# Kernel tuning notes

Measured on AMD Instinct MI355X. Metric: run time of the kernel, lower is better.

The kernel has to match this reference:

```python
import jax, jax.numpy as jnp
import numpy as np
import math

B, N, IN_DIM, EMBED, HEADS = 1, 96, 128, 128, 4
HD = EMBED // HEADS  # head_dim = 32


def _layernorm(x, g, b, eps=1e-5):
    mu = jnp.mean(x, axis=-1, keepdims=True)
    var = jnp.var(x, axis=-1, keepdims=True)
    return (x - mu) * jax.lax.rsqrt(var + eps) * g + b


def setup_inputs() -> dict:
    key = jax.random.key(0)
    ks = jax.random.split(key, 3)
    x = jax.random.normal(ks[0], (B, N, N, IN_DIM), dtype=jnp.float32)
    W = jax.random.normal(ks[1], (IN_DIM, EMBED), dtype=jnp.float32) / math.sqrt(IN_DIM)
    b = jnp.zeros((EMBED,), jnp.float32)
    ln_g = jnp.ones((HD,), jnp.float32)
    ln_b = jnp.zeros((HD,), jnp.float32)
    Wf = jax.random.normal(ks[2], (IN_DIM + EMBED, EMBED), dtype=jnp.float32) / math.sqrt(IN_DIM + EMBED)
    bf = jnp.zeros((EMBED,), jnp.float32)
    ln2_g = jnp.ones((EMBED,), jnp.float32)
    ln2_b = jnp.zeros((EMBED,), jnp.float32)
    return {"x": x, "W": W, "b": b, "ln_g": ln_g, "ln_b": ln_b,
            "Wf": Wf, "bf": bf, "ln2_g": ln2_g, "ln2_b": ln2_b}


def reference(x, W, b, ln_g, ln_b, Wf, bf, ln2_g, ln2_b):
    # NOTE: original torch module shares ONE Linear across q/k/v1/v2 and ONE
    # LayerNorm across norms[0..2] (ModuleList([m]*k) aliases the module).
    Bq, Nq = x.shape[0], x.shape[1]
    p = (jnp.einsum('bxyi,ie->bxye', x, W) + b).reshape(Bq, Nq, Nq, HEADS, HD)
    pn = _layernorm(p, ln_g, ln_b)                         # q == k (shared params)
    scores = jnp.einsum('bxahd,bayhd->bxayh', pn, pn) / math.sqrt(HD)
    att = jax.nn.softmax(scores, axis=2)                   # softmax over a
    x_upd = jnp.einsum('bxahd,bayhd->bxayhd', p, p)        # v1 == v2 == p
    x_upd = _layernorm(x_upd, ln_g, ln_b)                  # shared norm params
    agg = jnp.einsum('bxayh,bxayhd->bxyhd', att, x_upd).reshape(Bq, Nq, Nq, EMBED)
    cat = jnp.concatenate([x, agg], axis=-1)
    out = jnp.einsum('bxyc,ce->bxye', cat, Wf) + bf
    return _layernorm(out, ln2_g, ln2_b)
```

## Files before the change

kernel.cpp:

```cpp
#include <hip/hip_runtime.h>
#include <math.h>

#define NTOK 96
#define EMBED 128
#define HEADS 4
#define HD 32
#define NROW (NTOK*NTOK)
#define YT 8
#define NYT (NTOK/YT)

__global__ __launch_bounds__(128) void k_proj(
    const float* __restrict__ x, const float* __restrict__ W,
    const float* __restrict__ b,
    float* __restrict__ pT, float* __restrict__ murT) {
  const int r0 = blockIdx.x * 4;
  const int X  = r0 / NTOK;
  const int y0 = r0 % NTOK;
  const int e  = threadIdx.x;
  __shared__ float xt[EMBED][4];
  #pragma unroll
  for (int k = 0; k < 4; ++k)
    xt[e][k] = x[(size_t)(r0 + k) * EMBED + e];
  __syncthreads();

  const float bias = b[e];
  float a0 = bias, a1 = bias, a2 = bias, a3 = bias;
  #pragma unroll 8
  for (int i = 0; i < EMBED; ++i) {
    const float wv = W[(size_t)i * EMBED + e];
    const float4 c = *(const float4*)&xt[i][0];
    a0 = fmaf(wv, c.x, a0); a1 = fmaf(wv, c.y, a1);
    a2 = fmaf(wv, c.z, a2); a3 = fmaf(wv, c.w, a3);
  }

  const int h = e >> 5;
  float accs[4] = {a0, a1, a2, a3};
  #pragma unroll
  for (int k = 0; k < 4; ++k) {
    pT[((size_t)(y0 + k) * NTOK + X) * EMBED + e] = accs[k];
    float s1 = accs[k], s2 = accs[k] * accs[k];
    #pragma unroll
    for (int m_ = 1; m_ < 32; m_ <<= 1) {
      s1 += __shfl_xor(s1, m_, 64);
      s2 += __shfl_xor(s2, m_, 64);
    }
    if ((e & 31) == 0) {
      const float mu = s1 * (1.f / HD);
      const float var = fmaxf(s2 * (1.f / HD) - mu * mu, 0.f);
      float2 v; v.x = mu; v.y = rsqrtf(var + 1e-5f);
      *(float2*)&murT[(((size_t)(y0 + k) * NTOK + X) * HEADS + h) * 2] = v;
    }
  }
}

__device__ __forceinline__ void sc_elem(float e, float f, float g, float b,
    float rE, float pE, float rF, float pF,
    float& s, float& m, float& q, float& t) {
  const float uE = fmaf(e, rE, -pE);
  const float en = fmaf(uE, g, b);
  const float uF = fmaf(f, rF, -pF);
  const float fn = fmaf(uF, g, b);
  s = fmaf(en, fn, s);
  t = e * f;
  m += t;
  q = fmaf(t, t, q);
}

#define SC_QUAD(E4, F4, G4, B4, T4) \
  sc_elem(E4.x, F4.x, G4.x, B4.x, rE, pE, rF, pF, s, m, q, T4.x); \
  sc_elem(E4.y, F4.y, G4.y, B4.y, rE, pE, rF, pF, s, m, q, T4.y); \
  sc_elem(E4.z, F4.z, G4.z, B4.z, rE, pE, rF, pF, s, m, q, T4.z); \
  sc_elem(E4.w, F4.w, G4.w, B4.w, rE, pE, rF, pF, s, m, q, T4.w);

#define AGG_QUAD(A4, T4) \
  A4.x = fmaf(w, T4.x, A4.x); A4.y = fmaf(w, T4.y, A4.y); \
  A4.z = fmaf(w, T4.z, A4.z); A4.w = fmaf(w, T4.w, A4.w);

#define SCALE_QUAD(A4) \
  A4.x *= scale; A4.y *= scale; A4.z *= scale; A4.w *= scale;

#define RED_QUAD(A4, MASK) \
  A4.x += __shfl_xor(A4.x, MASK, 64); A4.y += __shfl_xor(A4.y, MASK, 64); \
  A4.z += __shfl_xor(A4.z, MASK, 64); A4.w += __shfl_xor(A4.w, MASK, 64);

__global__ __launch_bounds__(256) void k_fused(
    const float* __restrict__ pT, const float* __restrict__ murT,
    const float* __restrict__ ln_g, const float* __restrict__ ln_b,
    const float* __restrict__ x, const float* __restrict__ Wf,
    const float* __restrict__ bf, const float* __restrict__ g2,
    const float* __restrict__ b2, float* __restrict__ out) {
  const int bid = blockIdx.x;
  const int X   = bid % NTOK;
  const int y0  = (bid / NTOK) * YT;

  const int tid = threadIdx.x;
  const int y   = tid >> 5;
  const int ds  = (tid >> 4) & 1;
  const int da  = tid & 15;
  const int yy  = y0 + y;
  const int eoff = ds * 16;

  __shared__ float e_sm[NTOK][36];
  __shared__ float mur_sm[NTOK][2];
  __shared__ float xt_sm[EMBED][12];
  __shared__ float agg_t[EMBED][12];
  __shared__ float g_sm[HD], b_sm[HD];
  __shared__ float red_sm[4][4][2];

  #pragma unroll
  for (int i = 0; i < 4; ++i) {
    const int g = tid + i * 256;
    const int yl = g >> 7, col = g & 127;
    xt_sm[col][yl] = x[((size_t)(X * NTOK + y0 + yl)) * EMBED + col];
  }
  if (tid < HD) { g_sm[tid] = ln_g[tid]; b_sm[tid] = ln_b[tid]; }

  for (int H = 0; H < HEADS; ++H) {
    __syncthreads();
    #pragma unroll
    for (int i = 0; i < 3; ++i) {
      const int g = tid + i * 256;
      const int a = g >> 3, qq = g & 7;
      *(float4*)&e_sm[a][qq * 4] =
          *(const float4*)&pT[((size_t)a * NTOK + X) * EMBED + H * HD + qq * 4];
    }
    if (tid < NTOK) {
      const float2 v = *(const float2*)&murT[(((size_t)tid * NTOK + X) * HEADS + H) * 2];
      mur_sm[tid][0] = v.x; mur_sm[tid][1] = v.y;
    }
    __syncthreads();

    const float4 g0 = *(const float4*)&g_sm[eoff];
    const float4 g1 = *(const float4*)&g_sm[eoff + 4];
    const float4 g2v = *(const float4*)&g_sm[eoff + 8];
    const float4 g3 = *(const float4*)&g_sm[eoff + 12];
    const float4 b0 = *(const float4*)&b_sm[eoff];
    const float4 b1 = *(const float4*)&b_sm[eoff + 4];
    const float4 b2v = *(const float4*)&b_sm[eoff + 8];
    const float4 b3 = *(const float4*)&b_sm[eoff + 12];

    const float* fbase = pT + (size_t)yy * NTOK * EMBED + H * HD + eoff;
    const float* mbase = murT + ((size_t)yy * NTOK * HEADS + H) * 2;

    float4 acc0 = {0,0,0,0}, acc1 = {0,0,0,0}, acc2 = {0,0,0,0}, acc3 = {0,0,0,0};
    float den = 0.f, cc = 0.f, mx = -1e30f;

    #pragma unroll 2
    for (int ia = 0; ia < 6; ++ia) {
      const int a = ia * 16 + da;
      const float4* fp = (const float4*)(fbase + (size_t)a * EMBED);
      const float4 f0 = fp[0], f1 = fp[1], f2 = fp[2], f3 = fp[3];
      const float2 mrF = *(const float2*)(mbase + (size_t)a * (HEADS * 2));
      const float muE = mur_sm[a][0], rE = mur_sm[a][1];
      const float rF = mrF.y;
      const float pE = muE * rE;
      const float pF = mrF.x * rF;
      const float4 e0 = *(const float4*)&e_sm[a][eoff];
      const float4 e1 = *(const float4*)&e_sm[a][eoff + 4];
      const float4 e2 = *(const float4*)&e_sm[a][eoff + 8];
      const float4 e3 = *(const float4*)&e_sm[a][eoff + 12];

      float s = 0.f, m = 0.f, q = 0.f;
      float4 t0, t1, t2, t3;
      SC_QUAD(e0, f0, g0, b0, t0);
      SC_QUAD(e1, f1, g1, b1, t1);
      SC_QUAD(e2, f2, g2v, b2v, t2);
      SC_QUAD(e3, f3, g3, b3, t3);

      s += __shfl_xor(s, 16, 64);
      m += __shfl_xor(m, 16, 64);
      q += __shfl_xor(q, 16, 64);

      const float mu = m * (1.f / HD);
      const float var = fmaxf(fmaf(-mu, mu, q * (1.f / HD)), 0.f);
      const float r = rsqrtf(var + 1e-5f);
      const float sc = s * 0.17677669529663687f;

      float mc = sc;
      mc = fmaxf(mc, __shfl_xor(mc, 1, 64));
      mc = fmaxf(mc, __shfl_xor(mc, 2, 64));
      mc = fmaxf(mc, __shfl_xor(mc, 4, 64));
      mc = fmaxf(mc, __shfl_xor(mc, 8, 64));
      const float nmx = fmaxf(mx, mc);
      const float scale = __expf(mx - nmx);
      mx = nmx;
      const float ex = __expf(sc - mx);
      const float w = ex * r;
      den = fmaf(den, scale, ex);
      cc  = fmaf(cc,  scale, w * mu);
      SCALE_QUAD(acc0); SCALE_QUAD(acc1); SCALE_QUAD(acc2); SCALE_QUAD(acc3);
      AGG_QUAD(acc0, t0);
      AGG_QUAD(acc1, t1);
      AGG_QUAD(acc2, t2);
      AGG_QUAD(acc3, t3);
    }

    #pragma unroll
    for (int mask = 1; mask <= 8; mask <<= 1) {
      den += __shfl_xor(den, mask, 64);
      cc  += __shfl_xor(cc,  mask, 64);
      RED_QUAD(acc0, mask);
      RED_QUAD(acc1, mask);
      RED_QUAD(acc2, mask);
      RED_QUAD(acc3, mask);
    }

    if (da == 0) {
      const float inv = 1.f / den;
      float ov[16];
      ov[0]  = fmaf(g0.x, (acc0.x - cc) * inv, b0.x);
      ov[1]  = fmaf(g0.y, (acc0.y - cc) * inv, b0.y);
      ov[2]  = fmaf(g0.z, (acc0.z - cc) * inv, b0.z);
      ov[3]  = fmaf(g0.w, (acc0.w - cc) * inv, b0.w);
      ov[4]  = fmaf(g1.x, (acc1.x - cc) * inv, b1.x);
      ov[5]  = fmaf(g1.y, (acc1.y - cc) * inv, b1.y);
      ov[6]  = fmaf(g1.z, (acc1.z - cc) * inv, b1.z);
      ov[7]  = fmaf(g1.w, (acc1.w - cc) * inv, b1.w);
      ov[8]  = fmaf(g2v.x, (acc2.x - cc) * inv, b2v.x);
      ov[9]  = fmaf(g2v.y, (acc2.y - cc) * inv, b2v.y);
      ov[10] = fmaf(g2v.z, (acc2.z - cc) * inv, b2v.z);
      ov[11] = fmaf(g2v.w, (acc2.w - cc) * inv, b2v.w);
      ov[12] = fmaf(g3.x, (acc3.x - cc) * inv, b3.x);
      ov[13] = fmaf(g3.y, (acc3.y - cc) * inv, b3.y);
      ov[14] = fmaf(g3.z, (acc3.z - cc) * inv, b3.z);
      ov[15] = fmaf(g3.w, (acc3.w - cc) * inv, b3.w);
      #pragma unroll
      for (int j = 0; j < 16; ++j)
        agg_t[H * HD + eoff + j][y] = ov[j];
    }
  }
  __syncthreads();

  const int e  = tid & 127;
  const int rh = tid >> 7;
  const float bias = bf[e];
  float acc4[4] = {bias, bias, bias, bias};

  #pragma unroll 8
  for (int i = 0; i < EMBED; ++i) {
    const float wv = Wf[(size_t)i * EMBED + e];
    const float4 c0 = *(const float4*)&xt_sm[i][rh * 4];
    acc4[0] = fmaf(wv, c0.x, acc4[0]); acc4[1] = fmaf(wv, c0.y, acc4[1]);
    acc4[2] = fmaf(wv, c0.z, acc4[2]); acc4[3] = fmaf(wv, c0.w, acc4[3]);
  }
  #pragma unroll 8
  for (int i = 0; i < EMBED; ++i) {
    const float wv = Wf[(size_t)(EMBED + i) * EMBED + e];
    const float4 c0 = *(const float4*)&agg_t[i][rh * 4];
    acc4[0] = fmaf(wv, c0.x, acc4[0]); acc4[1] = fmaf(wv, c0.y, acc4[1]);
    acc4[2] = fmaf(wv, c0.z, acc4[2]); acc4[3] = fmaf(wv, c0.w, acc4[3]);
  }

  const int wid = tid >> 6;
  #pragma unroll
  for (int k = 0; k < 4; ++k) {
    float s1 = acc4[k], s2 = acc4[k] * acc4[k];
    #pragma unroll
    for (int m_ = 1; m_ < 64; m_ <<= 1) {
      s1 += __shfl_xor(s1, m_, 64);
      s2 += __shfl_xor(s2, m_, 64);
    }
    if ((tid & 63) == 0) { red_sm[wid][k][0] = s1; red_sm[wid][k][1] = s2; }
  }
  __syncthreads();

  const float gg = g2[e], bb = b2[e];
  #pragma unroll
  for (int k = 0; k < 4; ++k) {
    const float S1 = red_sm[wid][k][0] + red_sm[wid ^ 1][k][0];
    const float S2 = red_sm[wid][k][1] + red_sm[wid ^ 1][k][1];
    const float mu = S1 * (1.f / EMBED);
    const float var = fmaxf(S2 * (1.f / EMBED) - mu * mu, 0.f);
    const float rstd = rsqrtf(var + 1e-5f);
    out[((size_t)(X * NTOK + y0 + rh * 4 + k)) * EMBED + e] =
        (acc4[k] - mu) * rstd * gg + bb;
  }
}

extern "C" void kernel_launch(void* const* d_in, const int* in_sizes, int n_in,
                              void* d_out, int out_size, void* d_ws, size_t ws_size,
                              hipStream_t stream) {
  const float* x    = (const float*)d_in[0];
  const float* W    = (const float*)d_in[1];
  const float* b    = (const float*)d_in[2];
  const float* ln_g = (const float*)d_in[3];
  const float* ln_b = (const float*)d_in[4];
  const float* Wf   = (const float*)d_in[5];
  const float* bf   = (const float*)d_in[6];
  const float* g2   = (const float*)d_in[7];
  const float* b2   = (const float*)d_in[8];
  float* out = (float*)d_out;

  float* pT   = (float*)d_ws;
  float* murT = pT + (size_t)NROW * EMBED;

  k_proj<<<NROW / 4, 128, 0, stream>>>(x, W, b, pT, murT);
  k_fused<<<NTOK * NYT, 256, 0, stream>>>(pT, murT, ln_g, ln_b,
                                          x, Wf, bf, g2, b2, out);
}
```

Before: 108.4 us.

## Split fused kernel into per-head attention and final projection kernels, factor LN out of scores

The fused attention+projection kernel is split into k_attn, which now runs one head per block for four times more blocks, and k_final, which does the concatenated Wf projection plus LayerNorm from an agg buffer in global memory. The q·k score is rewritten algebraically so the per-element LayerNorm of both operands is replaced by a gamma-squared weighted raw dot product. The correction terms (sum g^2*v, sum g*b*v) are precomputed in k_proj and stored alongside mu and rstd as a float4. This cuts ALU work in the inner loop and improves parallelism. In exchange it adds a kernel launch, a global round trip for agg, and possible precision loss from the expanded-form score.

```diff
diff --git a/kernel.cpp b/kernel.cpp
--- a/kernel.cpp
+++ b/kernel.cpp
@@ -11,8 +11,9 @@
 
 __global__ __launch_bounds__(128) void k_proj(
     const float* __restrict__ x, const float* __restrict__ W,
-    const float* __restrict__ b,
-    float* __restrict__ pT, float* __restrict__ murT) {
+    const float* __restrict__ b, const float* __restrict__ ln_g,
+    const float* __restrict__ ln_b,
+    float* __restrict__ pT, float4* __restrict__ murT) {
   const int r0 = blockIdx.x * 4;
   const int X  = r0 / NTOK;
   const int y0 = r0 % NTOK;
@@ -34,43 +35,37 @@
   }
 
   const int h = e >> 5;
+  const float gl = ln_g[e & 31];
+  const float bl = ln_b[e & 31];
+  const float gl2 = gl * gl;
+  const float gvb = gl * bl;
   float accs[4] = {a0, a1, a2, a3};
   #pragma unroll
   for (int k = 0; k < 4; ++k) {
-    pT[((size_t)(y0 + k) * NTOK + X) * EMBED + e] = accs[k];
-    float s1 = accs[k], s2 = accs[k] * accs[k];
+    const float v = accs[k];
+    pT[((size_t)(y0 + k) * NTOK + X) * EMBED + e] = v;
+    float s1 = v, s2 = v * v, s3 = gl2 * v, s4 = gvb * v;
     #pragma unroll
     for (int m_ = 1; m_ < 32; m_ <<= 1) {
       s1 += __shfl_xor(s1, m_, 64);
       s2 += __shfl_xor(s2, m_, 64);
+      s3 += __shfl_xor(s3, m_, 64);
+      s4 += __shfl_xor(s4, m_, 64);
     }
     if ((e & 31) == 0) {
       const float mu = s1 * (1.f / HD);
       const float var = fmaxf(s2 * (1.f / HD) - mu * mu, 0.f);
-      float2 v; v.x = mu; v.y = rsqrtf(var + 1e-5f);
-      *(float2*)&murT[(((size_t)(y0 + k) * NTOK + X) * HEADS + h) * 2] = v;
+      float4 o; o.x = mu; o.y = rsqrtf(var + 1e-5f); o.z = s3; o.w = s4;
+      murT[((size_t)(y0 + k) * NTOK + X) * HEADS + h] = o;
     }
   }
 }
 
-__device__ __forceinline__ void sc_elem(float e, float f, float g, float b,
-    float rE, float pE, float rF, float pF,
-    float& s, float& m, float& q, float& t) {
-  const float uE = fmaf(e, rE, -pE);
-  const float en = fmaf(uE, g, b);
-  const float uF = fmaf(f, rF, -pF);
-  const float fn = fmaf(uF, g, b);
-  s = fmaf(en, fn, s);
-  t = e * f;
-  m += t;
-  q = fmaf(t, t, q);
-}
-
-#define SC_QUAD(E4, F4, G4, B4, T4) \
-  sc_elem(E4.x, F4.x, G4.x, B4.x, rE, pE, rF, pF, s, m, q, T4.x); \
-  sc_elem(E4.y, F4.y, G4.y, B4.y, rE, pE, rF, pF, s, m, q, T4.y); \
-  sc_elem(E4.z, F4.z, G4.z, B4.z, rE, pE, rF, pF, s, m, q, T4.z); \
-  sc_elem(E4.w, F4.w, G4.w, B4.w, rE, pE, rF, pF, s, m, q, T4.w);
+#define PR_QUAD(E4, F4, G2, T4) \
+  T4.x = E4.x * F4.x; sraw = fmaf(G2.x, T4.x, sraw); m += T4.x; q = fmaf(T4.x, T4.x, q); \
+  T4.y = E4.y * F4.y; sraw = fmaf(G2.y, T4.y, sraw); m += T4.y; q = fmaf(T4.y, T4.y, q); \
+  T4.z = E4.z * F4.z; sraw = fmaf(G2.z, T4.z, sraw); m += T4.z; q = fmaf(T4.z, T4.z, q); \
+  T4.w = E4.w * F4.w; sraw = fmaf(G2.w, T4.w, sraw); m += T4.w; q = fmaf(T4.w, T4.w, q);
 
 #define AGG_QUAD(A4, T4) \
   A4.x = fmaf(w, T4.x, A4.x); A4.y = fmaf(w, T4.y, A4.y); \
@@ -83,15 +78,15 @@
   A4.x += __shfl_xor(A4.x, MASK, 64); A4.y += __shfl_xor(A4.y, MASK, 64); \
   A4.z += __shfl_xor(A4.z, MASK, 64); A4.w += __shfl_xor(A4.w, MASK, 64);
 
-__global__ __launch_bounds__(256) void k_fused(
-    const float* __restrict__ pT, const float* __restrict__ murT,
+__global__ __launch_bounds__(256) void k_attn(
+    const float* __restrict__ pT, const float4* __restrict__ murT,
     const float* __restrict__ ln_g, const float* __restrict__ ln_b,
-    const float* __restrict__ x, const float* __restrict__ Wf,
-    const float* __restrict__ bf, const float* __restrict__ g2,
-    const float* __restrict__ b2, float* __restrict__ out) {
+    float* __restrict__ agg) {
   const int bid = blockIdx.x;
   const int X   = bid % NTOK;
-  const int y0  = (bid / NTOK) * YT;
+  const int t2i = bid / NTOK;
+  const int y0  = (t2i % NYT) * YT;
+  const int H   = t2i / NYT;
 
   const int tid = threadIdx.x;
   const int y   = tid >> 5;
@@ -101,152 +96,171 @@
   const int eoff = ds * 16;
 
   __shared__ float e_sm[NTOK][36];
-  __shared__ float mur_sm[NTOK][2];
-  __shared__ float xt_sm[EMBED][12];
-  __shared__ float agg_t[EMBED][12];
-  __shared__ float g_sm[HD], b_sm[HD];
+  __shared__ float4 mur_sm[NTOK];
+
+  #pragma unroll
+  for (int i = 0; i < 3; ++i) {
+    const int g = tid + i * 256;
+    const int a = g >> 3, qq = g & 7;
+    *(float4*)&e_sm[a][qq * 4] =
+        *(const float4*)&pT[((size_t)a * NTOK + X) * EMBED + H * HD + qq * 4];
+  }
+  if (tid < NTOK)
+    mur_sm[tid] = murT[((size_t)tid * NTOK + X) * HEADS + H];
+
+  {
+  }
+  const float glx = ln_g[tid & 31];
+  const float blx = ln_b[tid & 31];
+  float T2c = glx * glx, Vbc = glx * blx, Wbc = blx * blx;
+  #pragma unroll
+  for (int m_ = 1; m_ < 32; m_ <<= 1) {
+    T2c += __shfl_xor(T2c, m_, 64);
+    Vbc += __shfl_xor(Vbc, m_, 64);
+    Wbc += __shfl_xor(Wbc, m_, 64);
+  }
+  const float4 ga0 = *(const float4*)&ln_g[eoff];
+  const float4 ga1 = *(const float4*)&ln_g[eoff + 4];
+  const float4 ga2 = *(const float4*)&ln_g[eoff + 8];
+  const float4 ga3 = *(const float4*)&ln_g[eoff + 12];
+  float4 g2q0, g2q1, g2q2, g2q3;
+  g2q0.x = ga0.x*ga0.x; g2q0.y = ga0.y*ga0.y; g2q0.z = ga0.z*ga0.z; g2q0.w = ga0.w*ga0.w;
+  g2q1.x = ga1.x*ga1.x; g2q1.y = ga1.y*ga1.y; g2q1.z = ga1.z*ga1.z; g2q1.w = ga1.w*ga1.w;
+  g2q2.x = ga2.x*ga2.x; g2q2.y = ga2.y*ga2.y; g2q2.z = ga2.z*ga2.z; g2q2.w = ga2.w*ga2.w;
+  g2q3.x = ga3.x*ga3.x; g2q3.y = ga3.y*ga3.y; g2q3.z = ga3.z*ga3.z; g2q3.w = ga3.w*ga3.w;
+  __syncthreads();
+
+  const float* fbase = pT + (size_t)yy * NTOK * EMBED + H * HD + eoff;
+  const float4* mfb  = murT + (size_t)yy * NTOK * HEADS + H;
+
+  float4 acc0 = {0,0,0,0}, acc1 = {0,0,0,0}, acc2 = {0,0,0,0}, acc3 = {0,0,0,0};
+  float den = 0.f, cc = 0.f, mx = -1e30f;
+
+  #pragma unroll 2
+  for (int ia = 0; ia < 6; ++ia) {
+    const int a = ia * 16 + da;
+    const float4* fp = (const float4*)(fbase + (size_t)a * EMBED);
+    const float4 f0 = fp[0], f1 = fp[1], f2 = fp[2], f3 = fp[3];
+    const float4 mrF = mfb[(size_t)a * HEADS];
+    const float4 mrE = mur_sm[a];
+    const float4 e0 = *(const float4*)&e_sm[a][eoff];
+    const float4 e1 = *(const float4*)&e_sm[a][eoff + 4];
+    const float4 e2 = *(const float4*)&e_sm[a][eoff + 8];
+    const float4 e3 = *(const float4*)&e_sm[a][eoff + 12];
+
+    float sraw = 0.f, m = 0.f, q = 0.f;
+    float4 t0, t1, t2, t3;
+    PR_QUAD(e0, f0, g2q0, t0);
+    PR_QUAD(e1, f1, g2q1, t1);
+    PR_QUAD(e2, f2, g2q2, t2);
+    PR_QUAD(e3, f3, g2q3, t3);
+
+    sraw += __shfl_xor(sraw, 16, 64);
+    m    += __shfl_xor(m,    16, 64);
+    q    += __shfl_xor(q,    16, 64);
+
+    const float muE = mrE.x, rE = mrE.y, Sg2E = mrE.z, SgbE = mrE.w;
+    const float muF = mrF.x, rF = mrF.y, Sg2F = mrF.z, SgbF = mrF.w;
+    float inner = sraw - muF * Sg2E - muE * Sg2F + muE * muF * T2c;
+    float sfull = rE * rF * inner
+                + rE * (SgbE - muE * Vbc)
+                + rF * (SgbF - muF * Vbc) + Wbc;
+    const float sc = sfull * 0.17677669529663687f;
+
+    const float mu = m * (1.f / HD);
+    const float var = fmaxf(fmaf(-mu, mu, q * (1.f / HD)), 0.f);
+    const float r = rsqrtf(var + 1e-5f);
+
+    float mc = sc;
+    mc = fmaxf(mc, __shfl_xor(mc, 1, 64));
+    mc = fmaxf(mc, __shfl_xor(mc, 2, 64));
+    mc = fmaxf(mc, __shfl_xor(mc, 4, 64));
+    mc = fmaxf(mc, __shfl_xor(mc, 8, 64));
+    const float nmx = fmaxf(mx, mc);
+    const float scale = __expf(mx - nmx);
+    mx = nmx;
+    const float ex = __expf(sc - mx);
+    const float w = ex * r;
+    den = fmaf(den, scale, ex);
+    cc  = fmaf(cc,  scale, w * mu);
+    SCALE_QUAD(acc0); SCALE_QUAD(acc1); SCALE_QUAD(acc2); SCALE_QUAD(acc3);
+    AGG_QUAD(acc0, t0);
+    AGG_QUAD(acc1, t1);
+    AGG_QUAD(acc2, t2);
+    AGG_QUAD(acc3, t3);
+  }
+
+  #pragma unroll
+  for (int mask = 1; mask <= 8; mask <<= 1) {
+    den += __shfl_xor(den, mask, 64);
+    cc  += __shfl_xor(cc,  mask, 64);
+    RED_QUAD(acc0, mask);
+    RED_QUAD(acc1, mask);
+    RED_QUAD(acc2, mask);
+    RED_QUAD(acc3, mask);
+  }
+
+  if (da == 0) {
+    const float4 gq0 = ga0, gq1 = ga1, gq2 = ga2, gq3 = ga3;
+    const float4 bq0 = *(const float4*)&ln_b[eoff];
+    const float4 bq1 = *(const float4*)&ln_b[eoff + 4];
+    const float4 bq2 = *(const float4*)&ln_b[eoff + 8];
+    const float4 bq3 = *(const float4*)&ln_b[eoff + 12];
+    const float inv = 1.f / den;
+    float4 o0, o1, o2, o3;
+    o0.x = fmaf(gq0.x, (acc0.x - cc) * inv, bq0.x);
+    o0.y = fmaf(gq0.y, (acc0.y - cc) * inv, bq0.y);
+    o0.z = fmaf(gq0.z, (acc0.z - cc) * inv, bq0.z);
+    o0.w = fmaf(gq0.w, (acc0.w - cc) * inv, bq0.w);
+    o1.x = fmaf(gq1.x, (acc1.x - cc) * inv, bq1.x);
+    o1.y = fmaf(gq1.y, (acc1.y - cc) * inv, bq1.y);
+    o1.z = fmaf(gq1.z, (acc1.z - cc) * inv, bq1.z);
+    o1.w = fmaf(gq1.w, (acc1.w - cc) * inv, bq1.w);
+    o2.x = fmaf(gq2.x, (acc2.x - cc) * inv, bq2.x);
+    o2.y = fmaf(gq2.y, (acc2.y - cc) * inv, bq2.y);
+    o2.z = fmaf(gq2.z, (acc2.z - cc) * inv, bq2.z);
+    o2.w = fmaf(gq2.w, (acc2.w - cc) * inv, bq2.w);
+    o3.x = fmaf(gq3.x, (acc3.x - cc) * inv, bq3.x);
+    o3.y = fmaf(gq3.y, (acc3.y - cc) * inv, bq3.y);
+    o3.z = fmaf(gq3.z, (acc3.z - cc) * inv, bq3.z);
+    o3.w = fmaf(gq3.w, (acc3.w - cc) * inv, bq3.w);
+    float* op = agg + ((size_t)(X * NTOK + yy)) * EMBED + H * HD + eoff;
+    *(float4*)&op[0]  = o0;
+    *(float4*)&op[4]  = o1;
+    *(float4*)&op[8]  = o2;
+    *(float4*)&op[12] = o3;
+  }
+}
+
+__global__ __launch_bounds__(256) void k_final(
+    const float* __restrict__ x, const float* __restrict__ agg,
+    const float* __restrict__ Wf, const float* __restrict__ bf,
+    const float* __restrict__ g2, const float* __restrict__ b2,
+    float* __restrict__ out) {
+  const int r0 = blockIdx.x * 8;
+  const int tid = threadIdx.x;
+  const int e = tid & 127;
+  const int rh = tid >> 7;
+  __shared__ float ct[2 * EMBED][12];
   __shared__ float red_sm[4][4][2];
 
   #pragma unroll
-  for (int i = 0; i < 4; ++i) {
+  for (int i = 0; i < 8; ++i) {
     const int g = tid + i * 256;
-    const int yl = g >> 7, col = g & 127;
-    xt_sm[col][yl] = x[((size_t)(X * NTOK + y0 + yl)) * EMBED + col];
-  }
-  if (tid < HD) { g_sm[tid] = ln_g[tid]; b_sm[tid] = ln_b[tid]; }
-
-  for (int H = 0; H < HEADS; ++H) {
-    __syncthreads();
-    #pragma unroll
-    for (int i = 0; i < 3; ++i) {
-      const int g = tid + i * 256;
-      const int a = g >> 3, qq = g & 7;
-      *(float4*)&e_sm[a][qq * 4] =
-          *(const float4*)&pT[((size_t)a * NTOK + X) * EMBED + H * HD + qq * 4];
-    }
-    if (tid < NTOK) {
-      const float2 v = *(const float2*)&murT[(((size_t)tid * NTOK + X) * HEADS + H) * 2];
-      mur_sm[tid][0] = v.x; mur_sm[tid][1] = v.y;
-    }
-    __syncthreads();
-
-    const float4 g0 = *(const float4*)&g_sm[eoff];
-    const float4 g1 = *(const float4*)&g_sm[eoff + 4];
-    const float4 g2v = *(const float4*)&g_sm[eoff + 8];
-    const float4 g3 = *(const float4*)&g_sm[eoff + 12];
-    const float4 b0 = *(const float4*)&b_sm[eoff];
-    const float4 b1 = *(const float4*)&b_sm[eoff + 4];
-    const float4 b2v = *(const float4*)&b_sm[eoff + 8];
-    const float4 b3 = *(const float4*)&b_sm[eoff + 12];
-
-    const float* fbase = pT + (size_t)yy * NTOK * EMBED + H * HD + eoff;
-    const float* mbase = murT + ((size_t)yy * NTOK * HEADS + H) * 2;
-
-    float4 acc0 = {0,0,0,0}, acc1 = {0,0,0,0}, acc2 = {0,0,0,0}, acc3 = {0,0,0,0};
-    float den = 0.f, cc = 0.f, mx = -1e30f;
-
-    #pragma unroll 2
-    for (int ia = 0; ia < 6; ++ia) {
-      const int a = ia * 16 + da;
-      const float4* fp = (const float4*)(fbase + (size_t)a * EMBED);
-      const float4 f0 = fp[0], f1 = fp[1], f2 = fp[2], f3 = fp[3];
-      const float2 mrF = *(const float2*)(mbase + (size_t)a * (HEADS * 2));
-      const float muE = mur_sm[a][0], rE = mur_sm[a][1];
-      const float rF = mrF.y;
-      const float pE = muE * rE;
-      const float pF = mrF.x * rF;
-      const float4 e0 = *(const float4*)&e_sm[a][eoff];
-      const float4 e1 = *(const float4*)&e_sm[a][eoff + 4];
-      const float4 e2 = *(const float4*)&e_sm[a][eoff + 8];
-      const float4 e3 = *(const float4*)&e_sm[a][eoff + 12];
-
-      float s = 0.f, m = 0.f, q = 0.f;
-      float4 t0, t1, t2, t3;
-      SC_QUAD(e0, f0, g0, b0, t0);
-      SC_QUAD(e1, f1, g1, b1, t1);
-      SC_QUAD(e2, f2, g2v, b2v, t2);
-      SC_QUAD(e3, f3, g3, b3, t3);
-
-      s += __shfl_xor(s, 16, 64);
-      m += __shfl_xor(m, 16, 64);
-      q += __shfl_xor(q, 16, 64);
-
-      const float mu = m * (1.f / HD);
-      const float var = fmaxf(fmaf(-mu, mu, q * (1.f / HD)), 0.f);
-      const float r = rsqrtf(var + 1e-5f);
-      const float sc = s * 0.17677669529663687f;
-
-      float mc = sc;
-      mc = fmaxf(mc, __shfl_xor(mc, 1, 64));
-      mc = fmaxf(mc, __shfl_xor(mc, 2, 64));
-      mc = fmaxf(mc, __shfl_xor(mc, 4, 64));
-      mc = fmaxf(mc, __shfl_xor(mc, 8, 64));
-      const float nmx = fmaxf(mx, mc);
-      const float scale = __expf(mx - nmx);
-      mx = nmx;
-      const float ex = __expf(sc - mx);
-      const float w = ex * r;
-      den = fmaf(den, scale, ex);
-      cc  = fmaf(cc,  scale, w * mu);
-      SCALE_QUAD(acc0); SCALE_QUAD(acc1); SCALE_QUAD(acc2); SCALE_QUAD(acc3);
-      AGG_QUAD(acc0, t0);
-      AGG_QUAD(acc1, t1);
-      AGG_QUAD(acc2, t2);
-      AGG_QUAD(acc3, t3);
-    }
-
-    #pragma unroll
-    for (int mask = 1; mask <= 8; mask <<= 1) {
-      den += __shfl_xor(den, mask, 64);
-      cc  += __shfl_xor(cc,  mask, 64);
-      RED_QUAD(acc0, mask);
-      RED_QUAD(acc1, mask);
-      RED_QUAD(acc2, mask);
-      RED_QUAD(acc3, mask);
-    }
-
-    if (da == 0) {
-      const float inv = 1.f / den;
-      float ov[16];
-      ov[0]  = fmaf(g0.x, (acc0.x - cc) * inv, b0.x);
-      ov[1]  = fmaf(g0.y, (acc0.y - cc) * inv, b0.y);
-      ov[2]  = fmaf(g0.z, (acc0.z - cc) * inv, b0.z);
-      ov[3]  = fmaf(g0.w, (acc0.w - cc) * inv, b0.w);
-      ov[4]  = fmaf(g1.x, (acc1.x - cc) * inv, b1.x);
-      ov[5]  = fmaf(g1.y, (acc1.y - cc) * inv, b1.y);
-      ov[6]  = fmaf(g1.z, (acc1.z - cc) * inv, b1.z);
-      ov[7]  = fmaf(g1.w, (acc1.w - cc) * inv, b1.w);
-      ov[8]  = fmaf(g2v.x, (acc2.x - cc) * inv, b2v.x);
-      ov[9]  = fmaf(g2v.y, (acc2.y - cc) * inv, b2v.y);
-      ov[10] = fmaf(g2v.z, (acc2.z - cc) * inv, b2v.z);
-      ov[11] = fmaf(g2v.w, (acc2.w - cc) * inv, b2v.w);
-      ov[12] = fmaf(g3.x, (acc3.x - cc) * inv, b3.x);
-      ov[13] = fmaf(g3.y, (acc3.y - cc) * inv, b3.y);
-      ov[14] = fmaf(g3.z, (acc3.z - cc) * inv, b3.z);
-      ov[15] = fmaf(g3.w, (acc3.w - cc) * inv, b3.w);
-      #pragma unroll
-      for (int j = 0; j < 16; ++j)
-        agg_t[H * HD + eoff + j][y] = ov[j];
-    }
+    const int yl = g >> 8, col = g & 255;
+    const size_t row = (size_t)(r0 + yl);
+    const float v = (col < 128) ? x[row * EMBED + col]
+                                : agg[row * EMBED + (col - 128)];
+    ct[col][yl] = v;
   }
   __syncthreads();
 
-  const int e  = tid & 127;
-  const int rh = tid >> 7;
   const float bias = bf[e];
   float acc4[4] = {bias, bias, bias, bias};
-
   #pragma unroll 8
-  for (int i = 0; i < EMBED; ++i) {
+  for (int i = 0; i < 2 * EMBED; ++i) {
     const float wv = Wf[(size_t)i * EMBED + e];
-    const float4 c0 = *(const float4*)&xt_sm[i][rh * 4];
-    acc4[0] = fmaf(wv, c0.x, acc4[0]); acc4[1] = fmaf(wv, c0.y, acc4[1]);
-    acc4[2] = fmaf(wv, c0.z, acc4[2]); acc4[3] = fmaf(wv, c0.w, acc4[3]);
-  }
-  #pragma unroll 8
-  for (int i = 0; i < EMBED; ++i) {
-    const float wv = Wf[(size_t)(EMBED + i) * EMBED + e];
-    const float4 c0 = *(const float4*)&agg_t[i][rh * 4];
+    const float4 c0 = *(const float4*)&ct[i][rh * 4];
     acc4[0] = fmaf(wv, c0.x, acc4[0]); acc4[1] = fmaf(wv, c0.y, acc4[1]);
     acc4[2] = fmaf(wv, c0.z, acc4[2]); acc4[3] = fmaf(wv, c0.w, acc4[3]);
   }
@@ -272,8 +286,7 @@
     const float mu = S1 * (1.f / EMBED);
     const float var = fmaxf(S2 * (1.f / EMBED) - mu * mu, 0.f);
     const float rstd = rsqrtf(var + 1e-5f);
-    out[((size_t)(X * NTOK + y0 + rh * 4 + k)) * EMBED + e] =
-        (acc4[k] - mu) * rstd * gg + bb;
+    out[(size_t)(r0 + rh * 4 + k) * EMBED + e] = (acc4[k] - mu) * rstd * gg + bb;
   }
 }
 
@@ -291,10 +304,11 @@
   const float* b2   = (const float*)d_in[8];
   float* out = (float*)d_out;
 
-  float* pT   = (float*)d_ws;
-  float* murT = pT + (size_t)NROW * EMBED;
-
-  k_proj<<<NROW / 4, 128, 0, stream>>>(x, W, b, pT, murT);
-  k_fused<<<NTOK * NYT, 256, 0, stream>>>(pT, murT, ln_g, ln_b,
-                                          x, Wf, bf, g2, b2, out);
+  float*  pT   = (float*)d_ws;
+  float4* murT = (float4*)(pT + (size_t)NROW * EMBED);
+  float*  agg  = (float*)(murT + (size_t)NROW * HEADS);
+
+  k_proj<<<NROW / 4, 128, 0, stream>>>(x, W, b, ln_g, ln_b, pT, murT);
+  k_attn<<<NTOK * NYT * HEADS, 256, 0, stream>>>(pT, murT, ln_g, ln_b, agg);
+  k_final<<<NROW / 8, 256, 0, stream>>>(x, agg, Wf, bf, g2, b2, out);
 }
```

Measured after the change: 118.1 us. 8.9% more time.
